# Kernel tuning notes

Measured on AMD Instinct MI355X. Metric: run time of the kernel, lower is better.

The kernel has to match this reference:

```python
import jax, jax.numpy as jnp
import numpy as np

N_NODES = 50000
N_EDGES = 800000
C_IN = 64
C_OUT = 64
K = 3


def setup_inputs() -> dict:
    key = jax.random.key(0)
    k1, k2, k3, k4, k5, k6 = jax.random.split(key, 6)
    x = jax.random.normal(k1, (N_NODES, C_IN), dtype=jnp.float32)
    edge_index = jax.random.randint(k2, (2, N_EDGES), 0, N_NODES, dtype=jnp.int32)
    edge_weight = jax.random.uniform(k3, (N_EDGES,), dtype=jnp.float32)
    # Xavier-uniform init for [K, C_IN, C_OUT] (fan over last two dims)
    limit = float(np.sqrt(6.0 / (C_IN + C_OUT)))
    theta_forward = jax.random.uniform(k4, (K, C_IN, C_OUT), minval=-limit, maxval=limit, dtype=jnp.float32)
    theta_backward = jax.random.uniform(k5, (K, C_IN, C_OUT), minval=-limit, maxval=limit, dtype=jnp.float32)
    return {
        "x": x,
        "edge_index": edge_index,
        "edge_weight": edge_weight,
        "theta_forward": theta_forward,
        "theta_backward": theta_backward,
    }


def _propagate(x, row, col, edge_weight, n_nodes):
    # degree normalization: deg[i] = sum of edge_weight over edges with row == i
    deg = jax.ops.segment_sum(edge_weight, row, num_segments=n_nodes)
    deg_inv = jnp.where(deg > 0, jax.lax.rsqrt(jnp.where(deg > 0, deg, 1.0)), 0.0)
    norm = deg_inv[row] * edge_weight * deg_inv[col]      # [E]
    msg = norm[:, None] * x[col]                          # [E, C] gather-scale
    return jax.ops.segment_sum(msg, row, num_segments=n_nodes)  # scatter-add -> [N, C]


def reference(x, edge_index, edge_weight, theta_forward, theta_backward):
    row, col = edge_index[0], edge_index[1]
    n_nodes = x.shape[0]
    k = theta_forward.shape[0]
    Tx_0 = x
    Tx_1 = _propagate(x, row, col, edge_weight, n_nodes)
    out = Tx_0 @ theta_forward[0] + Tx_1 @ theta_backward[0]
    for i in range(1, k):
        Tx_2 = _propagate(Tx_1, row, col, edge_weight, n_nodes)
        out = out + Tx_2 @ theta_forward[i] + Tx_1 @ theta_backward[i]
        Tx_1 = Tx_2
    return out
```

## Files before the change

### kernel.cpp

```cpp
#include <hip/hip_runtime.h>
#include <hip/hip_fp16.h>


#define N_NODES 50000
#define N_EDGES 800000
#define C 64
#define CAP 64
#define NPART 196
#define CAPP 4608
#define EPB 8192
#define NEB 98
#define XH_BLOCKS 782
#define CW_BLOCKS 16

typedef _Float16 half8 __attribute__((ext_vector_type(8)));
typedef float f32x4 __attribute__((ext_vector_type(4)));

__global__ __launch_bounds__(1024) void scatter2_kernel(
        const int* __restrict__ row, const int* __restrict__ col,
        const float* __restrict__ w, int* __restrict__ percur,
        uint2* __restrict__ pedges,
        const float* __restrict__ x, __half* __restrict__ xh,
        const float* __restrict__ tf, const float* __restrict__ tb,
        _Float16* __restrict__ whc) {
    const int tid = threadIdx.x;
    if (blockIdx.x >= NEB + XH_BLOCKS) {
        int idx = (blockIdx.x - NEB - XH_BLOCKS) * 1024 + tid;
        int j = idx >> 12;
        int rem = idx & 4095;
        int ci = rem >> 6;
        int co = rem & 63;
        float v;
        if (j == 0)      v = tf[rem];
        else if (j == 1) v = tb[rem] + tb[4096 + rem];
        else if (j == 2) v = tf[4096 + rem] + tb[8192 + rem];
        else             v = tf[8192 + rem];
        whc[(j << 12) + (co << 6) + ci] = (_Float16)v;
        return;
    }
    if (blockIdx.x >= NEB) {
        int i = (blockIdx.x - NEB) * 1024 + tid;
        if (i < N_NODES * C / 4) {
            float4 v = ((const float4*)x)[i];
            union { float2 f2; __half2 h2[2]; } u;
            u.h2[0] = __floats2half2_rn(v.x, v.y);
            u.h2[1] = __floats2half2_rn(v.z, v.w);
            ((float2*)xh)[i] = u.f2;
        }
        return;
    }
    __shared__ int h[NPART];
    __shared__ int cur[NPART];
    uint2 ent[8];
    int pp[8];
    if (tid < NPART) h[tid] = 0;
    __syncthreads();
    int base = blockIdx.x * EPB;
#pragma unroll
    for (int i = 0; i < 8; ++i) {
        int e = base + i * 1024 + tid;
        pp[i] = -1;
        if (e < N_EDGES) {
            int r = row[e];
            unsigned int c = (unsigned int)col[e];
            unsigned int wh = (unsigned int)__half_as_ushort(__float2half_rn(w[e]));
            ent[i] = make_uint2((c << 16) | wh, (unsigned int)(r & 255));
            pp[i] = r >> 8;
            atomicAdd(&h[pp[i]], 1);
        }
    }
    __syncthreads();
    if (tid < NPART) cur[tid] = atomicAdd(&percur[tid], h[tid]);
    __syncthreads();
#pragma unroll
    for (int i = 0; i < 8; ++i) {
        if (pp[i] >= 0) {
            int slot = atomicAdd(&cur[pp[i]], 1);
            pedges[(size_t)pp[i] * CAPP + slot] = ent[i];
        }
    }
}

__global__ __launch_bounds__(1024) void build_kernel(
        const uint2* __restrict__ pedges, const int* __restrict__ percur,
        unsigned int* __restrict__ bkt, int* __restrict__ cnt,
        float* __restrict__ dinv) {
    __shared__ unsigned int lbuck[256 * CAP];
    __shared__ int lcnt[256];
    const int tid = threadIdx.x;
    const int p = blockIdx.x;
    if (tid < 256) lcnt[tid] = 0;
    __syncthreads();
    int e = min(percur[p], CAPP);
    const uint2* src = pedges + (size_t)p * CAPP;
    for (int i = tid; i < e; i += 1024) {
        uint2 en = src[i];
        int rl = (int)en.y;
        int slot = atomicAdd(&lcnt[rl], 1);
        if (slot < CAP) lbuck[(rl << 6) + slot] = en.x;
    }
    __syncthreads();
    if (tid < 256) {
        int m = min(lcnt[tid], CAP);
        int g = (p << 8) + tid;
        float sum = 0.f;
        for (int j = 0; j < m; ++j)
            sum += __half2float(__ushort_as_half(
                (unsigned short)(lbuck[(tid << 6) + j] & 0xFFFFu)));
        if (g < N_NODES) {
            cnt[g] = m;
            dinv[g] = (sum > 0.f) ? rsqrtf(sum) : 0.f;
        }
    }
    __syncthreads();
    const uint4* s4 = (const uint4*)lbuck;
    uint4* dst = (uint4*)(bkt + ((size_t)p << 14));
    for (int i = tid; i < 256 * CAP / 4; i += 1024) dst[i] = s4[i];
}

__global__ __launch_bounds__(256) void prop_kernel(
        const __half* __restrict__ xin, __half* __restrict__ xout,
        const int* __restrict__ cnt, const unsigned int* __restrict__ bkt,
        const float* __restrict__ dinv) {
    int wave = (blockIdx.x * blockDim.x + threadIdx.x) >> 6;
    int lane = threadIdx.x & 63;
    int q = lane >> 4;
    int ql = lane & 15;
    int node = (wave << 2) + q;
    if (node >= N_NODES) return;
    int m = min(cnt[node], CAP);
    int base = node << 6;
    int cj[4];
    float nj[4];
#pragma unroll
    for (int s = 0; s < 4; ++s) {
        int idx = (s << 4) + ql;
        cj[s] = 0;
        nj[s] = 0.f;
        if (idx < m) {
            unsigned int b = bkt[base + idx];
            int c = (int)(b >> 16);
            cj[s] = c << 6;
            nj[s] = __half2float(__ushort_as_half((unsigned short)(b & 0xFFFFu))) * dinv[c];
        }
    }
    float ax = 0.f, ay = 0.f, az = 0.f, aw = 0.f;
#pragma unroll
    for (int s = 0; s < 4; ++s) {
        int cb = s << 4;
        if (cb >= m) break;
        int rem = m - cb;
        if (rem > 16) rem = 16;
        int mm = (rem + 7) & ~7;
        for (int jo = 0; jo < mm; jo += 8) {
            int cs[8];
            float ns[8];
            float2 vs[8];
#pragma unroll
            for (int t = 0; t < 8; ++t) {
                cs[t] = __shfl(cj[s], (q << 4) + jo + t);
                ns[t] = __shfl(nj[s], (q << 4) + jo + t);
            }
#pragma unroll
            for (int t = 0; t < 8; ++t)
                vs[t] = *(const float2*)(xin + cs[t] + (ql << 2));
#pragma unroll
            for (int t = 0; t < 8; ++t) {
                const __half2* hp = (const __half2*)&vs[t];
                float2 a = __half22float2(hp[0]);
                float2 b = __half22float2(hp[1]);
                ax += ns[t] * a.x;
                ay += ns[t] * a.y;
                az += ns[t] * b.x;
                aw += ns[t] * b.y;
            }
        }
    }
    float dr = dinv[node];
    union { float2 f2; __half2 h2[2]; } u;
    u.h2[0] = __floats2half2_rn(dr * ax, dr * ay);
    u.h2[1] = __floats2half2_rn(dr * az, dr * aw);
    *(float2*)(xout + base + (ql << 2)) = u.f2;
}

__global__ __launch_bounds__(256) void gemm_mfma_kernel(
        const __half* __restrict__ x0, const __half* __restrict__ x1,
        const __half* __restrict__ x2, const __half* __restrict__ x3,
        const _Float16* __restrict__ whc, float* __restrict__ out) {
    const int tid = threadIdx.x;
    const int wv = tid >> 6;
    const int lane = tid & 63;
    const int quad = lane >> 4;
    const int l16 = lane & 15;
    const int mbase = (blockIdx.x << 6) + (wv << 4);
    const __half* srcs[4] = {x0, x1, x2, x3};
    f32x4 acc0 = {}, acc1 = {}, acc2 = {}, acc3 = {};
    const int arow = mbase + l16;
    const bool aok = arow < N_NODES;
    const size_t abase = ((size_t)arow << 6) + (quad << 3);
    const half8 zero8 = {};
#pragma unroll
    for (int j = 0; j < 4; ++j) {
        const __half* src = srcs[j];
#pragma unroll
        for (int kk = 0; kk < 64; kk += 32) {
            half8 af = aok ? *(const half8*)(const void*)(src + abase + kk) : zero8;
            const _Float16* wb = whc + (j << 12) + kk + (quad << 3);
            half8 b0 = *(const half8*)(const void*)(wb + ((0 * 16 + l16) << 6));
            half8 b1 = *(const half8*)(const void*)(wb + ((1 * 16 + l16) << 6));
            half8 b2 = *(const half8*)(const void*)(wb + ((2 * 16 + l16) << 6));
            half8 b3 = *(const half8*)(const void*)(wb + ((3 * 16 + l16) << 6));
            acc0 = __builtin_amdgcn_mfma_f32_16x16x32_f16(af, b0, acc0, 0, 0, 0);
            acc1 = __builtin_amdgcn_mfma_f32_16x16x32_f16(af, b1, acc1, 0, 0, 0);
            acc2 = __builtin_amdgcn_mfma_f32_16x16x32_f16(af, b2, acc2, 0, 0, 0);
            acc3 = __builtin_amdgcn_mfma_f32_16x16x32_f16(af, b3, acc3, 0, 0, 0);
        }
    }
#pragma unroll
    for (int i = 0; i < 4; ++i) {
        int r = mbase + (quad << 2) + i;
        if (r < N_NODES) {
            float* dst = out + ((size_t)r << 6) + l16;
            dst[0]  = acc0[i];
            dst[16] = acc1[i];
            dst[32] = acc2[i];
            dst[48] = acc3[i];
        }
    }
}

extern "C" void kernel_launch(void* const* d_in, const int* in_sizes, int n_in,
                              void* d_out, int out_size, void* d_ws, size_t ws_size,
                              hipStream_t stream) {
    const float* x  = (const float*)d_in[0];
    const int*   ei = (const int*)d_in[1];
    const float* ew = (const float*)d_in[2];
    const float* tf = (const float*)d_in[3];
    const float* tb = (const float*)d_in[4];
    float* out = (float*)d_out;

    const int* row = ei;
    const int* col = ei + N_EDGES;

    const int NROWS_PAD = NPART * 256;
    float* ws = (float*)d_ws;
    size_t off = 0;
    int*    percur = (int*)(ws + off); off += 256;
    uint2*  pedges = (uint2*)(ws + off); off += (size_t)NPART * CAPP * 2;
    unsigned int* bkt = (unsigned int*)(ws + off); off += (size_t)NROWS_PAD * CAP;
    int*    cnt  = (int*)(ws + off); off += NROWS_PAD;
    float*  dinv = ws + off; off += NROWS_PAD;
    __half* xh   = (__half*)(ws + off); off += (size_t)N_NODES * C / 2;
    __half* tA   = (__half*)(ws + off); off += (size_t)N_NODES * C / 2;
    __half* tB   = (__half*)(ws + off); off += (size_t)N_NODES * C / 2;
    __half* tC   = (__half*)(ws + off); off += (size_t)N_NODES * C / 2;
    _Float16* whc = (_Float16*)(ws + off); off += 4 * 64 * 64 / 2;

    hipMemsetAsync(percur, 0, NPART * sizeof(int), stream);

    scatter2_kernel<<<NEB + XH_BLOCKS + CW_BLOCKS, 1024, 0, stream>>>(
        row, col, ew, percur, pedges, x, xh, tf, tb, whc);
    build_kernel<<<NPART, 1024, 0, stream>>>(pedges, percur, bkt, cnt, dinv);

    const int PB = (N_NODES + 15) / 16;
    prop_kernel<<<PB, 256, 0, stream>>>(xh, tA, cnt, bkt, dinv);
    prop_kernel<<<PB, 256, 0, stream>>>(tA, tB, cnt, bkt, dinv);
    prop_kernel<<<PB, 256, 0, stream>>>(tB, tC, cnt, bkt, dinv);

    const int GB = (N_NODES + 63) / 64;
    gemm_mfma_kernel<<<GB, 256, 0, stream>>>(xh, tA, tB, tC, whc, out);
}
```

Before: 165.5 us.

## Fuse final GEMM into last propagation and cache normalized edge weights

The first propagation pass multiplies each edge weight by dinv[col] and writes the normalized half-precision weight back into the bucket array, so the later passes skip the dinv gather. The separate MFMA GEMM kernel is removed. The last propagation pass stages its output tile in shared memory and does the 16x64 output GEMM in place, reading the other three feature arrays from global memory. The scatter kernel also uses smaller edge blocks (2048 instead of 8192 edges per block) for more parallelism. Rounding the normalized weights to half adds precision loss, and the fused pass adds a block-wide barrier.

Measured after the change: 162.4 us. About the same (-1.8%).

```diff
diff --git a/kernel.cpp b/kernel.cpp
--- a/kernel.cpp
+++ b/kernel.cpp
@@ -8,8 +8,8 @@
 #define CAP 64
 #define NPART 196
 #define CAPP 4608
-#define EPB 8192
-#define NEB 98
+#define EPB 2048
+#define NEB 391
 #define XH_BLOCKS 782
 #define CW_BLOCKS 16
 
@@ -51,13 +51,13 @@
     }
     __shared__ int h[NPART];
     __shared__ int cur[NPART];
-    uint2 ent[8];
-    int pp[8];
+    uint2 ent[2];
+    int pp[2];
     if (tid < NPART) h[tid] = 0;
     __syncthreads();
     int base = blockIdx.x * EPB;
 #pragma unroll
-    for (int i = 0; i < 8; ++i) {
+    for (int i = 0; i < 2; ++i) {
         int e = base + i * 1024 + tid;
         pp[i] = -1;
         if (e < N_EDGES) {
@@ -73,7 +73,7 @@
     if (tid < NPART) cur[tid] = atomicAdd(&percur[tid], h[tid]);
     __syncthreads();
 #pragma unroll
-    for (int i = 0; i < 8; ++i) {
+    for (int i = 0; i < 2; ++i) {
         if (pp[i] >= 0) {
             int slot = atomicAdd(&cur[pp[i]], 1);
             pedges[(size_t)pp[i] * CAPP + slot] = ent[i];
@@ -118,16 +118,19 @@
     for (int i = tid; i < 256 * CAP / 4; i += 1024) dst[i] = s4[i];
 }
 
+template <bool FIXW, bool FUSE_GEMM>
 __global__ __launch_bounds__(256) void prop_kernel(
         const __half* __restrict__ xin, __half* __restrict__ xout,
-        const int* __restrict__ cnt, const unsigned int* __restrict__ bkt,
-        const float* __restrict__ dinv) {
-    int wave = (blockIdx.x * blockDim.x + threadIdx.x) >> 6;
-    int lane = threadIdx.x & 63;
-    int q = lane >> 4;
-    int ql = lane & 15;
-    int node = (wave << 2) + q;
-    if (node >= N_NODES) return;
+        const int* __restrict__ cnt, unsigned int* __restrict__ bkt,
+        const float* __restrict__ dinv,
+        const __half* __restrict__ x0, const __half* __restrict__ x1,
+        const _Float16* __restrict__ whc, float* __restrict__ out) {
+    const int tid = threadIdx.x;
+    const int wib = tid >> 6;
+    const int lane = tid & 63;
+    const int q = lane >> 4;
+    const int ql = lane & 15;
+    const int node = (blockIdx.x << 4) + (wib << 2) + q;
     int m = min(cnt[node], CAP);
     int base = node << 6;
     int cj[4];
@@ -141,7 +144,15 @@
             unsigned int b = bkt[base + idx];
             int c = (int)(b >> 16);
             cj[s] = c << 6;
-            nj[s] = __half2float(__ushort_as_half((unsigned short)(b & 0xFFFFu))) * dinv[c];
+            float wv = __half2float(__ushort_as_half((unsigned short)(b & 0xFFFFu)));
+            if constexpr (FIXW) {
+                float nn = wv * dinv[c];
+                nj[s] = nn;
+                bkt[base + idx] = ((unsigned int)c << 16) |
+                    (unsigned int)__half_as_ushort(__float2half_rn(nn));
+            } else {
+                nj[s] = wv;
+            }
         }
     }
     float ax = 0.f, ay = 0.f, az = 0.f, aw = 0.f;
@@ -180,51 +191,35 @@
     union { float2 f2; __half2 h2[2]; } u;
     u.h2[0] = __floats2half2_rn(dr * ax, dr * ay);
     u.h2[1] = __floats2half2_rn(dr * az, dr * aw);
-    *(float2*)(xout + base + (ql << 2)) = u.f2;
-}
-
-__global__ __launch_bounds__(256) void gemm_mfma_kernel(
-        const __half* __restrict__ x0, const __half* __restrict__ x1,
-        const __half* __restrict__ x2, const __half* __restrict__ x3,
-        const _Float16* __restrict__ whc, float* __restrict__ out) {
-    const int tid = threadIdx.x;
-    const int wv = tid >> 6;
-    const int lane = tid & 63;
-    const int quad = lane >> 4;
-    const int l16 = lane & 15;
-    const int mbase = (blockIdx.x << 6) + (wv << 4);
-    const __half* srcs[4] = {x0, x1, x2, x3};
-    f32x4 acc0 = {}, acc1 = {}, acc2 = {}, acc3 = {};
-    const int arow = mbase + l16;
-    const bool aok = arow < N_NODES;
-    const size_t abase = ((size_t)arow << 6) + (quad << 3);
-    const half8 zero8 = {};
-#pragma unroll
-    for (int j = 0; j < 4; ++j) {
-        const __half* src = srcs[j];
-#pragma unroll
-        for (int kk = 0; kk < 64; kk += 32) {
-            half8 af = aok ? *(const half8*)(const void*)(src + abase + kk) : zero8;
-            const _Float16* wb = whc + (j << 12) + kk + (quad << 3);
-            half8 b0 = *(const half8*)(const void*)(wb + ((0 * 16 + l16) << 6));
-            half8 b1 = *(const half8*)(const void*)(wb + ((1 * 16 + l16) << 6));
-            half8 b2 = *(const half8*)(const void*)(wb + ((2 * 16 + l16) << 6));
-            half8 b3 = *(const half8*)(const void*)(wb + ((3 * 16 + l16) << 6));
-            acc0 = __builtin_amdgcn_mfma_f32_16x16x32_f16(af, b0, acc0, 0, 0, 0);
-            acc1 = __builtin_amdgcn_mfma_f32_16x16x32_f16(af, b1, acc1, 0, 0, 0);
-            acc2 = __builtin_amdgcn_mfma_f32_16x16x32_f16(af, b2, acc2, 0, 0, 0);
-            acc3 = __builtin_amdgcn_mfma_f32_16x16x32_f16(af, b3, acc3, 0, 0, 0);
-        }
-    }
-#pragma unroll
-    for (int i = 0; i < 4; ++i) {
-        int r = mbase + (quad << 2) + i;
-        if (r < N_NODES) {
-            float* dst = out + ((size_t)r << 6) + l16;
-            dst[0]  = acc0[i];
-            dst[16] = acc1[i];
-            dst[32] = acc2[i];
-            dst[48] = acc3[i];
+    if constexpr (!FUSE_GEMM) {
+        *(float2*)(xout + ((size_t)node << 6) + (ql << 2)) = u.f2;
+    } else {
+        __shared__ _Float16 tcl[16 * 72];
+        *(float2*)(void*)&tcl[((wib << 2) + q) * 72 + (ql << 2)] = u.f2;
+        __syncthreads();
+        const int mbase = blockIdx.x << 4;
+        const __half* gsrc[3] = {x0, x1, xin};
+        const size_t abase = ((size_t)(mbase + ql) << 6) + (q << 3);
+        f32x4 acc = {};
+#pragma unroll
+        for (int j = 0; j < 4; ++j) {
+#pragma unroll
+            for (int kk = 0; kk < 64; kk += 32) {
+                half8 af;
+                if (j < 3)
+                    af = *(const half8*)(const void*)(gsrc[j] + abase + kk);
+                else
+                    af = *(const half8*)(const void*)&tcl[ql * 72 + (q << 3) + kk];
+                const _Float16* wb = whc + (j << 12) + (((wib << 4) + ql) << 6)
+                                         + (q << 3) + kk;
+                half8 bf = *(const half8*)(const void*)wb;
+                acc = __builtin_amdgcn_mfma_f32_16x16x32_f16(af, bf, acc, 0, 0, 0);
+            }
+        }
+#pragma unroll
+        for (int i = 0; i < 4; ++i) {
+            int r = mbase + (q << 2) + i;
+            out[((size_t)r << 6) + (wib << 4) + ql] = acc[i];
         }
     }
 }
@@ -262,11 +257,11 @@
         row, col, ew, percur, pedges, x, xh, tf, tb, whc);
     build_kernel<<<NPART, 1024, 0, stream>>>(pedges, percur, bkt, cnt, dinv);
 
-    const int PB = (N_NODES + 15) / 16;
-    prop_kernel<<<PB, 256, 0, stream>>>(xh, tA, cnt, bkt, dinv);
-    prop_kernel<<<PB, 256, 0, stream>>>(tA, tB, cnt, bkt, dinv);
-    prop_kernel<<<PB, 256, 0, stream>>>(tB, tC, cnt, bkt, dinv);
-
-    const int GB = (N_NODES + 63) / 64;
-    gemm_mfma_kernel<<<GB, 256, 0, stream>>>(xh, tA, tB, tC, whc, out);
-}
+    const int PB = N_NODES / 16;
+    prop_kernel<true,  false><<<PB, 256, 0, stream>>>(
+        xh, tA, cnt, bkt, dinv, nullptr, nullptr, nullptr, nullptr);
+    prop_kernel<false, false><<<PB, 256, 0, stream>>>(
+        tA, tB, cnt, bkt, dinv, nullptr, nullptr, nullptr, nullptr);
+    prop_kernel<false, true><<<PB, 256, 0, stream>>>(
+        tB, tC, cnt, bkt, dinv, xh, tA, whc, out);
+}
```

## Split feature tables into channel halves and cache pre-normalized edge weights

Applied to the files above, without the earlier changes.

Feature tables are stored as two 32-channel halves, and each propagation launch runs twice as many blocks, each handling one half. The goal is a smaller gather working set per pass so it fits better in cache. The first propagation also writes a second bucket array holding the col-normalized weight in fp16, so later passes skip the dinv[col] lookup. The build step now copies only the filled bucket slots. In exchange, edge metadata is read twice (once per half), and the fp16-rounded normalized weight adds some precision loss.

Measured after the change: 168.3 us. Within noise of the previous version (+1.7%).

```diff
diff --git a/kernel.cpp b/kernel.cpp
--- a/kernel.cpp
+++ b/kernel.cpp
@@ -12,6 +12,8 @@
 #define NEB 98
 #define XH_BLOCKS 782
 #define CW_BLOCKS 16
+#define PB 3125
+#define GB 782
 
 typedef _Float16 half8 __attribute__((ext_vector_type(8)));
 typedef float f32x4 __attribute__((ext_vector_type(4)));
@@ -20,7 +22,8 @@
         const int* __restrict__ row, const int* __restrict__ col,
         const float* __restrict__ w, int* __restrict__ percur,
         uint2* __restrict__ pedges,
-        const float* __restrict__ x, __half* __restrict__ xh,
+        const float* __restrict__ x, __half* __restrict__ xh0,
+        __half* __restrict__ xh1,
         const float* __restrict__ tf, const float* __restrict__ tb,
         _Float16* __restrict__ whc) {
     const int tid = threadIdx.x;
@@ -45,7 +48,11 @@
             union { float2 f2; __half2 h2[2]; } u;
             u.h2[0] = __floats2half2_rn(v.x, v.y);
             u.h2[1] = __floats2half2_rn(v.z, v.w);
-            ((float2*)xh)[i] = u.f2;
+            int node = i >> 4;
+            int ci0 = (i & 15) << 2;
+            __half* dst = (ci0 < 32) ? (xh0 + node * 32 + ci0)
+                                     : (xh1 + node * 32 + (ci0 - 32));
+            *(float2*)(void*)dst = u.f2;
         }
         return;
     }
@@ -113,21 +120,33 @@
         }
     }
     __syncthreads();
-    const uint4* s4 = (const uint4*)lbuck;
-    uint4* dst = (uint4*)(bkt + ((size_t)p << 14));
-    for (int i = tid; i < 256 * CAP / 4; i += 1024) dst[i] = s4[i];
-}
-
+    {
+        int r = tid >> 2;
+        int ch = tid & 3;
+        int m = min(lcnt[r], CAP);
+        const uint4* s4 = (const uint4*)&lbuck[r << 6];
+        uint4* dst = (uint4*)(bkt + (((size_t)(p << 8) + r) << 6));
+        for (int j = ch; (j << 2) < m; j += 4) dst[j] = s4[j];
+    }
+}
+
+template <bool FIRST>
 __global__ __launch_bounds__(256) void prop_kernel(
-        const __half* __restrict__ xin, __half* __restrict__ xout,
+        const __half* __restrict__ xin0, const __half* __restrict__ xin1,
+        __half* __restrict__ xout0, __half* __restrict__ xout1,
         const int* __restrict__ cnt, const unsigned int* __restrict__ bkt,
-        const float* __restrict__ dinv) {
-    int wave = (blockIdx.x * blockDim.x + threadIdx.x) >> 6;
-    int lane = threadIdx.x & 63;
-    int q = lane >> 4;
-    int ql = lane & 15;
-    int node = (wave << 2) + q;
-    if (node >= N_NODES) return;
+        unsigned int* __restrict__ bkt2, const float* __restrict__ dinv) {
+    const int bid = blockIdx.x;
+    const int h = (bid >= PB) ? 1 : 0;
+    const int tb = bid - (h ? PB : 0);
+    const __half* __restrict__ xin = h ? xin1 : xin0;
+    __half* __restrict__ xout = h ? xout1 : xout0;
+    const int tid = threadIdx.x;
+    const int wib = tid >> 6;
+    const int lane = tid & 63;
+    const int q = lane >> 4;
+    const int ql = lane & 15;
+    const int node = (tb << 4) + (wib << 2) + q;
     int m = min(cnt[node], CAP);
     int base = node << 6;
     int cj[4];
@@ -140,11 +159,20 @@
         if (idx < m) {
             unsigned int b = bkt[base + idx];
             int c = (int)(b >> 16);
-            cj[s] = c << 6;
-            nj[s] = __half2float(__ushort_as_half((unsigned short)(b & 0xFFFFu))) * dinv[c];
-        }
-    }
-    float ax = 0.f, ay = 0.f, az = 0.f, aw = 0.f;
+            cj[s] = c << 5;
+            float wv = __half2float(__ushort_as_half((unsigned short)(b & 0xFFFFu)));
+            if constexpr (FIRST) {
+                float nn = wv * dinv[c];
+                nj[s] = nn;
+                if (h == 0)
+                    bkt2[base + idx] = ((unsigned int)c << 16) |
+                        (unsigned int)__half_as_ushort(__float2half_rn(nn));
+            } else {
+                nj[s] = wv;
+            }
+        }
+    }
+    float ax = 0.f, ay = 0.f;
 #pragma unroll
     for (int s = 0; s < 4; ++s) {
         int cb = s << 4;
@@ -155,7 +183,7 @@
         for (int jo = 0; jo < mm; jo += 8) {
             int cs[8];
             float ns[8];
-            float2 vs[8];
+            float vs[8];
 #pragma unroll
             for (int t = 0; t < 8; ++t) {
                 cs[t] = __shfl(cj[s], (q << 4) + jo + t);
@@ -163,29 +191,25 @@
             }
 #pragma unroll
             for (int t = 0; t < 8; ++t)
-                vs[t] = *(const float2*)(xin + cs[t] + (ql << 2));
+                vs[t] = *(const float*)(xin + cs[t] + (ql << 1));
 #pragma unroll
             for (int t = 0; t < 8; ++t) {
-                const __half2* hp = (const __half2*)&vs[t];
-                float2 a = __half22float2(hp[0]);
-                float2 b = __half22float2(hp[1]);
+                float2 a = __half22float2(*(const __half2*)&vs[t]);
                 ax += ns[t] * a.x;
                 ay += ns[t] * a.y;
-                az += ns[t] * b.x;
-                aw += ns[t] * b.y;
             }
         }
     }
     float dr = dinv[node];
-    union { float2 f2; __half2 h2[2]; } u;
-    u.h2[0] = __floats2half2_rn(dr * ax, dr * ay);
-    u.h2[1] = __floats2half2_rn(dr * az, dr * aw);
-    *(float2*)(xout + base + (ql << 2)) = u.f2;
+    __half2 o = __floats2half2_rn(dr * ax, dr * ay);
+    *(__half2*)(xout + ((size_t)node << 5) + (ql << 1)) = o;
 }
 
 __global__ __launch_bounds__(256) void gemm_mfma_kernel(
-        const __half* __restrict__ x0, const __half* __restrict__ x1,
-        const __half* __restrict__ x2, const __half* __restrict__ x3,
+        const __half* __restrict__ x0l, const __half* __restrict__ x0h,
+        const __half* __restrict__ x1l, const __half* __restrict__ x1h,
+        const __half* __restrict__ x2l, const __half* __restrict__ x2h,
+        const __half* __restrict__ x3l, const __half* __restrict__ x3h,
         const _Float16* __restrict__ whc, float* __restrict__ out) {
     const int tid = threadIdx.x;
     const int wv = tid >> 6;
@@ -193,18 +217,19 @@
     const int quad = lane >> 4;
     const int l16 = lane & 15;
     const int mbase = (blockIdx.x << 6) + (wv << 4);
-    const __half* srcs[4] = {x0, x1, x2, x3};
+    const __half* slo[4] = {x0l, x1l, x2l, x3l};
+    const __half* shi[4] = {x0h, x1h, x2h, x3h};
     f32x4 acc0 = {}, acc1 = {}, acc2 = {}, acc3 = {};
     const int arow = mbase + l16;
     const bool aok = arow < N_NODES;
-    const size_t abase = ((size_t)arow << 6) + (quad << 3);
+    const size_t abase = ((size_t)arow << 5) + (quad << 3);
     const half8 zero8 = {};
 #pragma unroll
     for (int j = 0; j < 4; ++j) {
-        const __half* src = srcs[j];
 #pragma unroll
         for (int kk = 0; kk < 64; kk += 32) {
-            half8 af = aok ? *(const half8*)(const void*)(src + abase + kk) : zero8;
+            const __half* sp = (kk == 0) ? slo[j] : shi[j];
+            half8 af = aok ? *(const half8*)(const void*)(sp + abase) : zero8;
             const _Float16* wb = whc + (j << 12) + kk + (quad << 3);
             half8 b0 = *(const half8*)(const void*)(wb + ((0 * 16 + l16) << 6));
             half8 b1 = *(const half8*)(const void*)(wb + ((1 * 16 + l16) << 6));
@@ -243,30 +268,38 @@
     const int* col = ei + N_EDGES;
 
     const int NROWS_PAD = NPART * 256;
+    const size_t HALF_TBL = (size_t)N_NODES * 32 / 2;
     float* ws = (float*)d_ws;
     size_t off = 0;
     int*    percur = (int*)(ws + off); off += 256;
     uint2*  pedges = (uint2*)(ws + off); off += (size_t)NPART * CAPP * 2;
-    unsigned int* bkt = (unsigned int*)(ws + off); off += (size_t)NROWS_PAD * CAP;
+    unsigned int* bkt  = (unsigned int*)(ws + off); off += (size_t)NROWS_PAD * CAP;
+    unsigned int* bkt2 = (unsigned int*)(ws + off); off += (size_t)NROWS_PAD * CAP;
     int*    cnt  = (int*)(ws + off); off += NROWS_PAD;
     float*  dinv = ws + off; off += NROWS_PAD;
-    __half* xh   = (__half*)(ws + off); off += (size_t)N_NODES * C / 2;
-    __half* tA   = (__half*)(ws + off); off += (size_t)N_NODES * C / 2;
-    __half* tB   = (__half*)(ws + off); off += (size_t)N_NODES * C / 2;
-    __half* tC   = (__half*)(ws + off); off += (size_t)N_NODES * C / 2;
+    __half* xh0 = (__half*)(ws + off); off += HALF_TBL;
+    __half* xh1 = (__half*)(ws + off); off += HALF_TBL;
+    __half* tA0 = (__half*)(ws + off); off += HALF_TBL;
+    __half* tA1 = (__half*)(ws + off); off += HALF_TBL;
+    __half* tB0 = (__half*)(ws + off); off += HALF_TBL;
+    __half* tB1 = (__half*)(ws + off); off += HALF_TBL;
+    __half* tC0 = (__half*)(ws + off); off += HALF_TBL;
+    __half* tC1 = (__half*)(ws + off); off += HALF_TBL;
     _Float16* whc = (_Float16*)(ws + off); off += 4 * 64 * 64 / 2;
 
-    hipMemsetAsync(percur, 0, NPART * sizeof(int), stream);
+    hipMemsetAsync(percur, 0, 256 * sizeof(int), stream);
 
     scatter2_kernel<<<NEB + XH_BLOCKS + CW_BLOCKS, 1024, 0, stream>>>(
-        row, col, ew, percur, pedges, x, xh, tf, tb, whc);
+        row, col, ew, percur, pedges, x, xh0, xh1, tf, tb, whc);
     build_kernel<<<NPART, 1024, 0, stream>>>(pedges, percur, bkt, cnt, dinv);
 
-    const int PB = (N_NODES + 15) / 16;
-    prop_kernel<<<PB, 256, 0, stream>>>(xh, tA, cnt, bkt, dinv);
-    prop_kernel<<<PB, 256, 0, stream>>>(tA, tB, cnt, bkt, dinv);
-    prop_kernel<<<PB, 256, 0, stream>>>(tB, tC, cnt, bkt, dinv);
-
-    const int GB = (N_NODES + 63) / 64;
-    gemm_mfma_kernel<<<GB, 256, 0, stream>>>(xh, tA, tB, tC, whc, out);
-}
+    prop_kernel<true><<<2 * PB, 256, 0, stream>>>(
+        xh0, xh1, tA0, tA1, cnt, bkt, bkt2, dinv);
+    prop_kernel<false><<<2 * PB, 256, 0, stream>>>(
+        tA0, tA1, tB0, tB1, cnt, bkt2, bkt2, dinv);
+    prop_kernel<false><<<2 * PB, 256, 0, stream>>>(
+        tB0, tB1, tC0, tC1, cnt, bkt2, bkt2, dinv);
+
+    gemm_mfma_kernel<<<GB, 256, 0, stream>>>(
+        xh0, xh1, tA0, tA1, tB0, tB1, tC0, tC1, whc, out);
+}
```

## Slice feature tables into 16-channel planes and predecode edge norms

Applied to the files above, without the earlier changes.

Feature tables are stored as four 16-channel slices per node, so each propagation block handles one slice and its gather working set is a quarter the size, which should fit better in cache. A new decode kernel folds dinv[col] into the stored edge weight once, so the three propagation passes no longer gather dinv per edge. Propagation now has each quad of lanes cover different edges and reduces with cross-lane shuffles. The build copy only writes occupied bucket entries. The cost is one extra kernel, an extra bucket array, four times as many propagation blocks that each re-read the edge lists, and an extra fp16 rounding of the combined norm.

After: 190.1 us. 14.9% more time.

```diff
diff --git a/kernel.cpp b/kernel.cpp
--- a/kernel.cpp
+++ b/kernel.cpp
@@ -12,6 +12,10 @@
 #define NEB 98
 #define XH_BLOCKS 782
 #define CW_BLOCKS 16
+#define NPADL 50176
+#define NSLICE 4
+#define PB 3125
+#define GB 782
 
 typedef _Float16 half8 __attribute__((ext_vector_type(8)));
 typedef float f32x4 __attribute__((ext_vector_type(4)));
@@ -45,7 +49,12 @@
             union { float2 f2; __half2 h2[2]; } u;
             u.h2[0] = __floats2half2_rn(v.x, v.y);
             u.h2[1] = __floats2half2_rn(v.z, v.w);
-            ((float2*)xh)[i] = u.f2;
+            int node = i >> 4;
+            int ci0 = (i & 15) << 2;
+            int slice = ci0 >> 4;
+            int off = ci0 & 15;
+            *(float2*)(void*)(xh + (((size_t)slice * NPADL + node) << 4) + off)
+                = u.f2;
         }
         return;
     }
@@ -113,23 +122,48 @@
         }
     }
     __syncthreads();
-    const uint4* s4 = (const uint4*)lbuck;
-    uint4* dst = (uint4*)(bkt + ((size_t)p << 14));
-    for (int i = tid; i < 256 * CAP / 4; i += 1024) dst[i] = s4[i];
+    {
+        int r = tid >> 2;
+        int ch = tid & 3;
+        int m = min(lcnt[r], CAP);
+        const uint4* s4 = (const uint4*)&lbuck[r << 6];
+        uint4* dst = (uint4*)(bkt + (((size_t)(p << 8) + r) << 6));
+        for (int j = ch; (j << 2) < m; j += 4) dst[j] = s4[j];
+    }
+}
+
+__global__ __launch_bounds__(1024) void decode_kernel(
+        const unsigned int* __restrict__ bkt, const int* __restrict__ cnt,
+        const float* __restrict__ dinv, unsigned int* __restrict__ bkt2) {
+    int e = blockIdx.x * 1024 + threadIdx.x;
+    int node = e >> 6;
+    int j = e & 63;
+    if (node < N_NODES && j < min(cnt[node], CAP)) {
+        unsigned int b = bkt[e];
+        int c = (int)(b >> 16);
+        float nn = __half2float(__ushort_as_half((unsigned short)(b & 0xFFFFu)))
+                   * dinv[c];
+        bkt2[e] = ((unsigned int)c << 16) |
+                  (unsigned int)__half_as_ushort(__float2half_rn(nn));
+    }
 }
 
 __global__ __launch_bounds__(256) void prop_kernel(
         const __half* __restrict__ xin, __half* __restrict__ xout,
-        const int* __restrict__ cnt, const unsigned int* __restrict__ bkt,
+        const int* __restrict__ cnt, const unsigned int* __restrict__ bkt2,
         const float* __restrict__ dinv) {
-    int wave = (blockIdx.x * blockDim.x + threadIdx.x) >> 6;
-    int lane = threadIdx.x & 63;
-    int q = lane >> 4;
-    int ql = lane & 15;
-    int node = (wave << 2) + q;
-    if (node >= N_NODES) return;
-    int m = min(cnt[node], CAP);
-    int base = node << 6;
+    const int tid = threadIdx.x;
+    const int wib = tid >> 6;
+    const int lane = tid & 63;
+    const int q = lane >> 4;
+    const int ql = lane & 15;
+    const int u = ql >> 2;
+    const int cq = ql & 3;
+    const int slice = blockIdx.x & 3;
+    const int tile = blockIdx.x >> 2;
+    const int node = (tile << 4) + (wib << 2) + q;
+    const int m = min(cnt[node], CAP);
+    const int base = node << 6;
     int cj[4];
     float nj[4];
 #pragma unroll
@@ -138,49 +172,52 @@
         cj[s] = 0;
         nj[s] = 0.f;
         if (idx < m) {
-            unsigned int b = bkt[base + idx];
-            int c = (int)(b >> 16);
-            cj[s] = c << 6;
-            nj[s] = __half2float(__ushort_as_half((unsigned short)(b & 0xFFFFu))) * dinv[c];
-        }
-    }
-    float ax = 0.f, ay = 0.f, az = 0.f, aw = 0.f;
+            unsigned int b = bkt2[base + idx];
+            cj[s] = (int)(b >> 16) << 4;
+            nj[s] = __half2float(__ushort_as_half((unsigned short)(b & 0xFFFFu)));
+        }
+    }
+    const __half* xsl = xin + ((size_t)slice * NPADL << 4);
+    float a0 = 0.f, a1 = 0.f, a2 = 0.f, a3 = 0.f;
 #pragma unroll
     for (int s = 0; s < 4; ++s) {
         int cb = s << 4;
         if (cb >= m) break;
-        int rem = m - cb;
-        if (rem > 16) rem = 16;
-        int mm = (rem + 7) & ~7;
-        for (int jo = 0; jo < mm; jo += 8) {
-            int cs[8];
-            float ns[8];
-            float2 vs[8];
-#pragma unroll
-            for (int t = 0; t < 8; ++t) {
-                cs[t] = __shfl(cj[s], (q << 4) + jo + t);
-                ns[t] = __shfl(nj[s], (q << 4) + jo + t);
-            }
-#pragma unroll
-            for (int t = 0; t < 8; ++t)
-                vs[t] = *(const float2*)(xin + cs[t] + (ql << 2));
-#pragma unroll
-            for (int t = 0; t < 8; ++t) {
-                const __half2* hp = (const __half2*)&vs[t];
-                float2 a = __half22float2(hp[0]);
-                float2 b = __half22float2(hp[1]);
-                ax += ns[t] * a.x;
-                ay += ns[t] * a.y;
-                az += ns[t] * b.x;
-                aw += ns[t] * b.y;
-            }
-        }
-    }
-    float dr = dinv[node];
-    union { float2 f2; __half2 h2[2]; } u;
-    u.h2[0] = __floats2half2_rn(dr * ax, dr * ay);
-    u.h2[1] = __floats2half2_rn(dr * az, dr * aw);
-    *(float2*)(xout + base + (ql << 2)) = u.f2;
+        int cs[4];
+        float ns[4];
+        float2 vs[4];
+#pragma unroll
+        for (int t = 0; t < 4; ++t) {
+            int sl = (q << 4) + (t << 2) + u;
+            cs[t] = __shfl(cj[s], sl);
+            ns[t] = __shfl(nj[s], sl);
+        }
+#pragma unroll
+        for (int t = 0; t < 4; ++t)
+            vs[t] = *(const float2*)(xsl + cs[t] + (cq << 2));
+#pragma unroll
+        for (int t = 0; t < 4; ++t) {
+            const __half2* hp = (const __half2*)&vs[t];
+            float2 A = __half22float2(hp[0]);
+            float2 B = __half22float2(hp[1]);
+            a0 += ns[t] * A.x;
+            a1 += ns[t] * A.y;
+            a2 += ns[t] * B.x;
+            a3 += ns[t] * B.y;
+        }
+    }
+    a0 += __shfl_xor(a0, 4); a0 += __shfl_xor(a0, 8);
+    a1 += __shfl_xor(a1, 4); a1 += __shfl_xor(a1, 8);
+    a2 += __shfl_xor(a2, 4); a2 += __shfl_xor(a2, 8);
+    a3 += __shfl_xor(a3, 4); a3 += __shfl_xor(a3, 8);
+    if (u == 0) {
+        float dr = dinv[node];
+        union { float2 f2; __half2 h2[2]; } o;
+        o.h2[0] = __floats2half2_rn(dr * a0, dr * a1);
+        o.h2[1] = __floats2half2_rn(dr * a2, dr * a3);
+        *(float2*)(void*)(xout + (((size_t)slice * NPADL + node) << 4)
+                          + (cq << 2)) = o.f2;
+    }
 }
 
 __global__ __launch_bounds__(256) void gemm_mfma_kernel(
@@ -197,14 +234,17 @@
     f32x4 acc0 = {}, acc1 = {}, acc2 = {}, acc3 = {};
     const int arow = mbase + l16;
     const bool aok = arow < N_NODES;
-    const size_t abase = ((size_t)arow << 6) + (quad << 3);
     const half8 zero8 = {};
 #pragma unroll
     for (int j = 0; j < 4; ++j) {
         const __half* src = srcs[j];
 #pragma unroll
         for (int kk = 0; kk < 64; kk += 32) {
-            half8 af = aok ? *(const half8*)(const void*)(src + abase + kk) : zero8;
+            const int k0 = kk + (quad << 3);
+            const int slice = k0 >> 4;
+            const int koff = k0 & 15;
+            half8 af = aok ? *(const half8*)(const void*)(
+                src + (((size_t)slice * NPADL + arow) << 4) + koff) : zero8;
             const _Float16* wb = whc + (j << 12) + kk + (quad << 3);
             half8 b0 = *(const half8*)(const void*)(wb + ((0 * 16 + l16) << 6));
             half8 b1 = *(const half8*)(const void*)(wb + ((1 * 16 + l16) << 6));
@@ -242,31 +282,31 @@
     const int* row = ei;
     const int* col = ei + N_EDGES;
 
-    const int NROWS_PAD = NPART * 256;
+    const size_t TBL = (size_t)NSLICE * NPADL * 16 / 2;
     float* ws = (float*)d_ws;
     size_t off = 0;
     int*    percur = (int*)(ws + off); off += 256;
     uint2*  pedges = (uint2*)(ws + off); off += (size_t)NPART * CAPP * 2;
-    unsigned int* bkt = (unsigned int*)(ws + off); off += (size_t)NROWS_PAD * CAP;
-    int*    cnt  = (int*)(ws + off); off += NROWS_PAD;
-    float*  dinv = ws + off; off += NROWS_PAD;
-    __half* xh   = (__half*)(ws + off); off += (size_t)N_NODES * C / 2;
-    __half* tA   = (__half*)(ws + off); off += (size_t)N_NODES * C / 2;
-    __half* tB   = (__half*)(ws + off); off += (size_t)N_NODES * C / 2;
-    __half* tC   = (__half*)(ws + off); off += (size_t)N_NODES * C / 2;
+    unsigned int* bkt  = (unsigned int*)(ws + off); off += (size_t)NPADL * CAP;
+    unsigned int* bkt2 = (unsigned int*)(ws + off); off += (size_t)NPADL * CAP;
+    int*    cnt  = (int*)(ws + off); off += NPADL;
+    float*  dinv = ws + off; off += NPADL;
+    __half* xh   = (__half*)(ws + off); off += TBL;
+    __half* tA   = (__half*)(ws + off); off += TBL;
+    __half* tB   = (__half*)(ws + off); off += TBL;
+    __half* tC   = (__half*)(ws + off); off += TBL;
     _Float16* whc = (_Float16*)(ws + off); off += 4 * 64 * 64 / 2;
 
-    hipMemsetAsync(percur, 0, NPART * sizeof(int), stream);
+    hipMemsetAsync(percur, 0, 256 * sizeof(int), stream);
 
     scatter2_kernel<<<NEB + XH_BLOCKS + CW_BLOCKS, 1024, 0, stream>>>(
         row, col, ew, percur, pedges, x, xh, tf, tb, whc);
     build_kernel<<<NPART, 1024, 0, stream>>>(pedges, percur, bkt, cnt, dinv);
-
-    const int PB = (N_NODES + 15) / 16;
-    prop_kernel<<<PB, 256, 0, stream>>>(xh, tA, cnt, bkt, dinv);
-    prop_kernel<<<PB, 256, 0, stream>>>(tA, tB, cnt, bkt, dinv);
-    prop_kernel<<<PB, 256, 0, stream>>>(tB, tC, cnt, bkt, dinv);
-
-    const int GB = (N_NODES + 63) / 64;
+    decode_kernel<<<NPADL * CAP / 1024, 1024, 0, stream>>>(bkt, cnt, dinv, bkt2);
+
+    prop_kernel<<<NSLICE * PB, 256, 0, stream>>>(xh, tA, cnt, bkt2, dinv);
+    prop_kernel<<<NSLICE * PB, 256, 0, stream>>>(tA, tB, cnt, bkt2, dinv);
+    prop_kernel<<<NSLICE * PB, 256, 0, stream>>>(tB, tC, cnt, bkt2, dinv);
+
     gemm_mfma_kernel<<<GB, 256, 0, stream>>>(xh, tA, tB, tC, whc, out);
 }
```
